# Performance work log

Hardware: AMD Instinct MI355X
Metric: run time of the kernel (lower is better)

The kernel has to match this reference:

```python
import jax, jax.numpy as jnp
import numpy as np

N = 50000
E = 800000
IN_C = 256
HID = 256
OUT_C = 128


def _glorot(key, fan_in, fan_out):
    lim = float(np.sqrt(6.0 / (fan_in + fan_out)))
    return jax.random.uniform(key, (fan_in, fan_out), jnp.float32, -lim, lim)


def setup_inputs() -> dict:
    key = jax.random.key(0)
    ks = jax.random.split(key, 10)
    x = jax.random.normal(ks[0], (N, IN_C), dtype=jnp.float32)
    edge_index = jax.random.randint(ks[1], (2, E), 0, N, dtype=jnp.int64)
    return {
        "x": x,
        "edge_index": edge_index,
        # layer 0 MLP: Linear(IN_C,HID)+ReLU+Linear(HID,HID)+ReLU
        "eps0": jnp.zeros((), jnp.float32),
        "W1_0": _glorot(ks[2], IN_C, HID),
        "b1_0": jnp.zeros((HID,), jnp.float32),
        "W2_0": _glorot(ks[3], HID, HID),
        "b2_0": jnp.zeros((HID,), jnp.float32),
        # layer 1 MLP: Linear(HID,HID)+ReLU+Linear(HID,OUT_C)
        "eps1": jnp.zeros((), jnp.float32),
        "W1_1": _glorot(ks[4], HID, HID),
        "b1_1": jnp.zeros((HID,), jnp.float32),
        "W2_1": _glorot(ks[5], HID, OUT_C),
        "b2_1": jnp.zeros((OUT_C,), jnp.float32),
    }


def _gin_layer(x, src, dst, eps, W1, b1, W2, b2, final_relu):
    # sum-aggregate messages x[src] into dst nodes
    agg = jax.ops.segment_sum(x[src], dst, num_segments=N)  # [N, d]
    h = (1.0 + eps) * x + agg
    h = jax.nn.relu(h @ W1 + b1)
    h = h @ W2 + b2
    return jax.nn.relu(h) if final_relu else h


def reference(x, edge_index, eps0, W1_0, b1_0, W2_0, b2_0, eps1, W1_1, b1_1, W2_1, b2_1):
    src, dst = edge_index[0], edge_index[1]
    h = _gin_layer(x, src, dst, eps0, W1_0, b1_0, W2_0, b2_0, final_relu=True)
    h = jax.nn.relu(h)  # model-level ReLU between layers
    h = _gin_layer(h, src, dst, eps1, W1_1, b1_1, W2_1, b2_1, final_relu=False)
    return jax.nn.log_softmax(h, axis=1)
```

## Files before the change

### kernel.cpp

```cpp
#include <hip/hip_runtime.h>

#define FDIM 256
#define OUTC 128
#define CAP  96
#define CURS 16
#define LDA 264
#define MROWS 64

typedef float floatx4 __attribute__((ext_vector_type(4)));
typedef __bf16 bf16x8 __attribute__((ext_vector_type(8)));

__device__ __forceinline__ unsigned short f2bf(float f) {
    union { float f; unsigned u; } v; v.f = f;
    unsigned r = v.u + 0x7FFF + ((v.u >> 16) & 1);
    return (unsigned short)(r >> 16);
}
__device__ __forceinline__ unsigned pack2(float a, float b) {
    return ((unsigned)f2bf(a)) | (((unsigned)f2bf(b)) << 16);
}
__device__ __forceinline__ unsigned q8b(float v, float rs) {
    int q = __float2int_rn(v * rs);
    q = (q < -127 ? -127 : (q > 127 ? 127 : q)) + 128;
    return (unsigned)q;
}
__device__ __forceinline__ float ub0(unsigned v) { float f; asm("v_cvt_f32_ubyte0 %0, %1" : "=v"(f) : "v"(v)); return f; }
__device__ __forceinline__ float ub1(unsigned v) { float f; asm("v_cvt_f32_ubyte1 %0, %1" : "=v"(f) : "v"(v)); return f; }
__device__ __forceinline__ float ub2(unsigned v) { float f; asm("v_cvt_f32_ubyte2 %0, %1" : "=v"(f) : "v"(v)); return f; }
__device__ __forceinline__ float ub3(unsigned v) { float f; asm("v_cvt_f32_ubyte3 %0, %1" : "=v"(f) : "v"(v)); return f; }

__device__ __forceinline__ void gl2lds16(const void* g, void* l) {
    __builtin_amdgcn_global_load_lds(
        (const __attribute__((address_space(1))) unsigned int*)g,
        (__attribute__((address_space(3))) unsigned int*)l, 16, 0, 0);
}

__global__ __launch_bounds__(256)
void prep_kernel(const int* __restrict__ src, const int* __restrict__ dst,
                 int* __restrict__ cursor, unsigned short* __restrict__ esrc2, int E,
                 const float* __restrict__ x, unsigned char* __restrict__ xq,
                 float* __restrict__ xs0, int total8,
                 const float* __restrict__ W1_0, const float* __restrict__ W2_0,
                 const float* __restrict__ W1_1, const float* __restrict__ W2_1,
                 unsigned short* __restrict__ w1f_0, unsigned short* __restrict__ w2f_0,
                 unsigned short* __restrict__ w1f_1, unsigned short* __restrict__ w2f_1) {
    int gid = blockIdx.x * 256 + threadIdx.x;
    if (gid < E) {
        int d = dst[gid];
        int pos = atomicAdd(&cursor[d * CURS], 1);
        if (pos < CAP) esrc2[d * CAP + pos] = (unsigned short)src[gid];
        return;
    }
    gid -= E;
    if (gid < total8) {
        const float4* p = (const float4*)(x + (size_t)gid * 8);
        float4 a = p[0], b = p[1];
        float m = fmaxf(fmaxf(fmaxf(fabsf(a.x), fabsf(a.y)), fmaxf(fabsf(a.z), fabsf(a.w))),
                        fmaxf(fmaxf(fabsf(b.x), fabsf(b.y)), fmaxf(fabsf(b.z), fabsf(b.w))));
        #pragma unroll
        for (int off = 1; off < 32; off <<= 1) m = fmaxf(m, __shfl_xor(m, off));
        float rs = (m > 0.f) ? 127.0f / m : 0.f;
        unsigned lo = q8b(a.x, rs) | (q8b(a.y, rs) << 8) |
                      (q8b(a.z, rs) << 16) | (q8b(a.w, rs) << 24);
        unsigned hi = q8b(b.x, rs) | (q8b(b.y, rs) << 8) |
                      (q8b(b.z, rs) << 16) | (q8b(b.w, rs) << 24);
        *(uint2*)(xq + (size_t)gid * 8) = make_uint2(lo, hi);
        if ((threadIdx.x & 31) == 0) xs0[gid >> 5] = m * (1.0f / 127.0f);
        return;
    }
    gid -= total8;
    const int S = FDIM * FDIM;
    const float* W; unsigned short* WF; int local, J, Ncols;
    if (gid < S)          { W = W1_0; WF = w1f_0; local = gid;         J = 4; Ncols = FDIM; }
    else if (gid < 2 * S) { W = W2_0; WF = w2f_0; local = gid - S;     J = 4; Ncols = FDIM; }
    else if (gid < 3 * S) { W = W1_1; WF = w1f_1; local = gid - 2 * S; J = 4; Ncols = FDIM; }
    else if (gid < 3 * S + FDIM * OUTC)
                          { W = W2_1; WF = w2f_1; local = gid - 3 * S; J = 2; Ncols = OUTC; }
    else return;
    int e    = local & 7;
    int lane = (local >> 3) & 63;
    int l15  = lane & 15;
    int quad = lane >> 4;
    int t  = local >> 9;
    int j  = t % J;  t /= J;
    int g  = t & 3;
    int kc = t >> 2;
    int n = g * (16 * J) + j * 16 + l15;
    int k = kc * 32 + quad * 8 + e;
    WF[local] = f2bf(W[(size_t)k * Ncols + n]);
}

__global__ __launch_bounds__(256)
void gather_q8_kernel(const unsigned char* __restrict__ q,
                      const float* __restrict__ qs,
                      const unsigned short* __restrict__ esrc2,
                      const int* __restrict__ cursor,
                      const float* __restrict__ epsp,
                      unsigned short* __restrict__ out, int N, float bias) {
    int node = __builtin_amdgcn_readfirstlane(
        (int)((blockIdx.x * blockDim.x + threadIdx.x) >> 6));
    int lane = threadIdx.x & 63;
    if (node >= N) return;
    int col = lane * 4;
    int beg = node * CAP;
    int cnt = cursor[node * CURS];
    if (cnt > CAP) cnt = CAP;

    float a4[4] = {0.f, 0.f, 0.f, 0.f};
    float scl_sum = 0.f;

    int e = 0;
    for (; e + 16 <= cnt; e += 16) {
        const uint4* ip = (const uint4*)(esrc2 + beg + e);
        uint4 i0 = ip[0], i1 = ip[1];
        unsigned iw[8] = {i0.x, i0.y, i0.z, i0.w, i1.x, i1.y, i1.z, i1.w};
        int s[16]; float sc[16];
        #pragma unroll
        for (int m = 0; m < 8; ++m) {
            s[2*m]   = __builtin_amdgcn_readfirstlane((int)(iw[m] & 0xffffu));
            s[2*m+1] = __builtin_amdgcn_readfirstlane((int)(iw[m] >> 16));
        }
        #pragma unroll
        for (int k = 0; k < 16; ++k) { sc[k] = qs[s[k]]; scl_sum += sc[k]; }
        unsigned v[16];
        #pragma unroll
        for (int k = 0; k < 16; ++k)
            v[k] = *(const unsigned*)(q + (size_t)s[k] * FDIM + col);
        #pragma unroll
        for (int k = 0; k < 16; ++k) {
            a4[0] = fmaf(sc[k], ub0(v[k]), a4[0]);
            a4[1] = fmaf(sc[k], ub1(v[k]), a4[1]);
            a4[2] = fmaf(sc[k], ub2(v[k]), a4[2]);
            a4[3] = fmaf(sc[k], ub3(v[k]), a4[3]);
        }
    }
    int rem = cnt - e;
    if (rem > 0) {
        const uint4* ip = (const uint4*)(esrc2 + beg + e);
        uint4 i0 = ip[0], i1 = ip[1];
        unsigned iw[8] = {i0.x, i0.y, i0.z, i0.w, i1.x, i1.y, i1.z, i1.w};
        int s[16]; float sc[16];
        #pragma unroll
        for (int m = 0; m < 8; ++m) {
            s[2*m]   = __builtin_amdgcn_readfirstlane((int)(iw[m] & 0xffffu));
            s[2*m+1] = __builtin_amdgcn_readfirstlane((int)(iw[m] >> 16));
        }
        #pragma unroll
        for (int k = 0; k < 16; ++k) if (k >= rem) s[k] = s[0];
        #pragma unroll
        for (int k = 0; k < 16; ++k) {
            sc[k] = (k < rem) ? qs[s[k]] : 0.f;
            scl_sum += sc[k];
        }
        unsigned v[16];
        #pragma unroll
        for (int k = 0; k < 16; ++k)
            v[k] = *(const unsigned*)(q + (size_t)s[k] * FDIM + col);
        #pragma unroll
        for (int k = 0; k < 16; ++k) {
            a4[0] = fmaf(sc[k], ub0(v[k]), a4[0]);
            a4[1] = fmaf(sc[k], ub1(v[k]), a4[1]);
            a4[2] = fmaf(sc[k], ub2(v[k]), a4[2]);
            a4[3] = fmaf(sc[k], ub3(v[k]), a4[3]);
        }
    }

    float ssc = qs[node] * (1.0f + *epsp);
    scl_sum += ssc;
    unsigned sv = *(const unsigned*)(q + (size_t)node * FDIM + col);
    a4[0] = fmaf(ssc, ub0(sv), a4[0]);
    a4[1] = fmaf(ssc, ub1(sv), a4[1]);
    a4[2] = fmaf(ssc, ub2(sv), a4[2]);
    a4[3] = fmaf(ssc, ub3(sv), a4[3]);

    float corr = bias * scl_sum;
    a4[0] -= corr; a4[1] -= corr; a4[2] -= corr; a4[3] -= corr;

    uint2 o;
    o.x = pack2(a4[0], a4[1]);
    o.y = pack2(a4[2], a4[3]);
    *(uint2*)(out + (size_t)node * FDIM + col) = o;
}

template<bool FINAL>
__global__ __launch_bounds__(256, 2)
void mlp_fused_kernel(const unsigned short* __restrict__ A,
                      const unsigned short* __restrict__ W1F,
                      const float* __restrict__ b1,
                      const unsigned short* __restrict__ W2F,
                      const float* __restrict__ b2,
                      void* __restrict__ Out,
                      float* __restrict__ xsp, int M) {
    __shared__ unsigned short As[MROWS * LDA];
    __shared__ unsigned short Bs[2][8192];
    __shared__ float sred[MROWS * 4 * 2];

    int tid  = threadIdx.x;
    int wave = tid >> 6;
    int lane = tid & 63;
    int l15  = lane & 15;
    int quad = lane >> 4;
    int row0 = blockIdx.x * MROWS;

    auto stageB = [&](const unsigned short* WF, int kcs, int buf, int sliceB) {
        const char* gs = (const char*)WF + (size_t)kcs * sliceB;
        char* ls = (char*)Bs[buf];
        int myg = wave * 1024 + lane * 16;
        int myl = wave * 1024;
        for (int r = 0; r < (sliceB >> 12); ++r)
            gl2lds16(gs + r * 4096 + myg, ls + r * 4096 + myl);
    };

    #pragma unroll
    for (int i = 0; i < 8; ++i) {
        int idx = i * 256 + tid;
        int r = idx >> 5;
        int c = (idx & 31) * 8;
        uint4 v = make_uint4(0u, 0u, 0u, 0u);
        int gr = row0 + r;
        if (gr < M) v = *(const uint4*)(A + (size_t)gr * FDIM + c);
        *(uint4*)(As + r * LDA + c) = v;
    }
    int cur = 0;
    stageB(W1F, 0, 0, 16384);
    asm volatile("s_waitcnt vmcnt(0)" ::: "memory");
    __syncthreads();

    floatx4 zero = {0.f, 0.f, 0.f, 0.f};

    {
        floatx4 acc[4][4];
        #pragma unroll
        for (int i = 0; i < 4; ++i)
            #pragma unroll
            for (int j = 0; j < 4; ++j) acc[i][j] = zero;

        for (int kc = 0; kc < 8; ++kc) {
            if (kc < 7) stageB(W1F, kc + 1, cur ^ 1, 16384);
            const unsigned short* Bc = Bs[cur] + wave * 2048;
            bf16x8 bf[4], af[4];
            #pragma unroll
            for (int j = 0; j < 4; ++j)
                bf[j] = *(const bf16x8*)(Bc + j * 512 + lane * 8);
            int k = kc * 32;
            #pragma unroll
            for (int i = 0; i < 4; ++i)
                af[i] = *(const bf16x8*)(As + (i * 16 + l15) * LDA + k + quad * 8);
            #pragma unroll
            for (int i = 0; i < 4; ++i)
                #pragma unroll
                for (int j = 0; j < 4; ++j)
                    acc[i][j] = __builtin_amdgcn_mfma_f32_16x16x32_bf16(
                        af[i], bf[j], acc[i][j], 0, 0, 0);
            asm volatile("s_waitcnt vmcnt(0)" ::: "memory");
            __syncthreads();
            cur ^= 1;
        }

        stageB(W2F, 0, cur, FINAL ? 8192 : 16384);

        #pragma unroll
        for (int j = 0; j < 4; ++j) {
            int col = wave * 64 + j * 16 + l15;
            float bv = b1[col];
            #pragma unroll
            for (int i = 0; i < 4; ++i) {
                #pragma unroll
                for (int r = 0; r < 4; ++r) {
                    float v = fmaxf(acc[i][j][r] + bv, 0.f);
                    As[(i * 16 + quad * 4 + r) * LDA + col] = f2bf(v);
                }
            }
        }
    }
    asm volatile("s_waitcnt vmcnt(0)" ::: "memory");
    __syncthreads();

    if (!FINAL) {
        floatx4 acc[4][4];
        #pragma unroll
        for (int i = 0; i < 4; ++i)
            #pragma unroll
            for (int j = 0; j < 4; ++j) acc[i][j] = zero;

        for (int kc = 0; kc < 8; ++kc) {
            if (kc < 7) stageB(W2F, kc + 1, cur ^ 1, 16384);
            const unsigned short* Bc = Bs[cur] + wave * 2048;
            bf16x8 bf[4], af[4];
            #pragma unroll
            for (int j = 0; j < 4; ++j)
                bf[j] = *(const bf16x8*)(Bc + j * 512 + lane * 8);
            int k = kc * 32;
            #pragma unroll
            for (int i = 0; i < 4; ++i)
                af[i] = *(const bf16x8*)(As + (i * 16 + l15) * LDA + k + quad * 8);
            #pragma unroll
            for (int i = 0; i < 4; ++i)
                #pragma unroll
                for (int j = 0; j < 4; ++j)
                    acc[i][j] = __builtin_amdgcn_mfma_f32_16x16x32_bf16(
                        af[i], bf[j], acc[i][j], 0, 0, 0);
            asm volatile("s_waitcnt vmcnt(0)" ::: "memory");
            __syncthreads();
            cur ^= 1;
        }

        #pragma unroll
        for (int j = 0; j < 4; ++j) {
            float bv = b2[wave * 64 + j * 16 + l15];
            #pragma unroll
            for (int i = 0; i < 4; ++i)
                #pragma unroll
                for (int r = 0; r < 4; ++r)
                    acc[i][j][r] = fmaxf(acc[i][j][r] + bv, 0.f);
        }
        #pragma unroll
        for (int i = 0; i < 4; ++i) {
            #pragma unroll
            for (int r = 0; r < 4; ++r) {
                float m = fmaxf(fmaxf(acc[i][0][r], acc[i][1][r]),
                                fmaxf(acc[i][2][r], acc[i][3][r]));
                #pragma unroll
                for (int off = 1; off < 16; off <<= 1) m = fmaxf(m, __shfl_xor(m, off));
                int row = i * 16 + quad * 4 + r;
                if (l15 == 0) sred[row * 4 + wave] = m;
            }
        }
        __syncthreads();

        unsigned char* Bq = (unsigned char*)As;
        #pragma unroll
        for (int i = 0; i < 4; ++i) {
            #pragma unroll
            for (int r = 0; r < 4; ++r) {
                int row = i * 16 + quad * 4 + r;
                float Mr = fmaxf(fmaxf(sred[row * 4 + 0], sred[row * 4 + 1]),
                                 fmaxf(sred[row * 4 + 2], sred[row * 4 + 3]));
                float rs = (Mr > 0.f) ? 255.0f / Mr : 0.f;
                if (wave == 0 && l15 == 0 && row0 + row < M)
                    xsp[row0 + row] = Mr * (1.0f / 255.0f);
                #pragma unroll
                for (int j = 0; j < 4; ++j) {
                    int col = wave * 64 + j * 16 + l15;
                    Bq[row * FDIM + col] =
                        (unsigned char)__float2int_rn(acc[i][j][r] * rs);
                }
            }
        }
        __syncthreads();

        unsigned char* Oq = (unsigned char*)Out;
        #pragma unroll
        for (int it = 0; it < 4; ++it) {
            int u4 = it * 256 + tid;
            int r = u4 >> 4;
            int gr = row0 + r;
            if (gr < M) {
                uint4 v = *(uint4*)(Bq + u4 * 16);
                *(uint4*)(Oq + (size_t)gr * FDIM + (u4 & 15) * 16) = v;
            }
        }
    } else {
        floatx4 acc[4][2];
        #pragma unroll
        for (int i = 0; i < 4; ++i)
            #pragma unroll
            for (int j = 0; j < 2; ++j) acc[i][j] = zero;

        for (int kc = 0; kc < 8; ++kc) {
            if (kc < 7) stageB(W2F, kc + 1, cur ^ 1, 8192);
            const unsigned short* Bc = Bs[cur] + wave * 1024;
            bf16x8 bf[2], af[4];
            #pragma unroll
            for (int j = 0; j < 2; ++j)
                bf[j] = *(const bf16x8*)(Bc + j * 512 + lane * 8);
            int k = kc * 32;
            #pragma unroll
            for (int i = 0; i < 4; ++i)
                af[i] = *(const bf16x8*)(As + (i * 16 + l15) * LDA + k + quad * 8);
            #pragma unroll
            for (int i = 0; i < 4; ++i)
                #pragma unroll
                for (int j = 0; j < 2; ++j)
                    acc[i][j] = __builtin_amdgcn_mfma_f32_16x16x32_bf16(
                        af[i], bf[j], acc[i][j], 0, 0, 0);
            asm volatile("s_waitcnt vmcnt(0)" ::: "memory");
            __syncthreads();
            cur ^= 1;
        }

        #pragma unroll
        for (int j = 0; j < 2; ++j) {
            float bv = b2[wave * 32 + j * 16 + l15];
            #pragma unroll
            for (int i = 0; i < 4; ++i)
                #pragma unroll
                for (int r = 0; r < 4; ++r) acc[i][j][r] += bv;
        }

        float* smax = sred;
        float* ssum = sred + MROWS * 4;

        #pragma unroll
        for (int i = 0; i < 4; ++i) {
            #pragma unroll
            for (int r = 0; r < 4; ++r) {
                float m = fmaxf(acc[i][0][r], acc[i][1][r]);
                #pragma unroll
                for (int off = 1; off < 16; off <<= 1) m = fmaxf(m, __shfl_xor(m, off));
                int row = i * 16 + quad * 4 + r;
                if (l15 == 0) smax[row * 4 + wave] = m;
            }
        }
        __syncthreads();

        float Mloc[4][4];
        #pragma unroll
        for (int i = 0; i < 4; ++i) {
            #pragma unroll
            for (int r = 0; r < 4; ++r) {
                int row = i * 16 + quad * 4 + r;
                float Mr = fmaxf(fmaxf(smax[row * 4 + 0], smax[row * 4 + 1]),
                                 fmaxf(smax[row * 4 + 2], smax[row * 4 + 3]));
                Mloc[i][r] = Mr;
                float s = __expf(acc[i][0][r] - Mr) + __expf(acc[i][1][r] - Mr);
                #pragma unroll
                for (int off = 1; off < 16; off <<= 1) s += __shfl_xor(s, off);
                if (l15 == 0) ssum[row * 4 + wave] = s;
            }
        }
        __syncthreads();

        float* O = (float*)Out;
        #pragma unroll
        for (int i = 0; i < 4; ++i) {
            #pragma unroll
            for (int r = 0; r < 4; ++r) {
                int row = i * 16 + quad * 4 + r;
                int grow = row0 + row;
                if (grow < M) {
                    float lse = Mloc[i][r] +
                        __logf(ssum[row * 4 + 0] + ssum[row * 4 + 1] +
                               ssum[row * 4 + 2] + ssum[row * 4 + 3]);
                    #pragma unroll
                    for (int j = 0; j < 2; ++j) {
                        int col = wave * 32 + j * 16 + l15;
                        O[(size_t)grow * OUTC + col] = acc[i][j][r] - lse;
                    }
                }
            }
        }
    }
}

extern "C" void kernel_launch(void* const* d_in, const int* in_sizes, int n_in,
                              void* d_out, int out_size, void* d_ws, size_t ws_size,
                              hipStream_t stream) {
    const float* x    = (const float*)d_in[0];
    const int*   ei   = (const int*)d_in[1];
    const float* eps0 = (const float*)d_in[2];
    const float* W1_0 = (const float*)d_in[3];
    const float* b1_0 = (const float*)d_in[4];
    const float* W2_0 = (const float*)d_in[5];
    const float* b2_0 = (const float*)d_in[6];
    const float* eps1 = (const float*)d_in[7];
    const float* W1_1 = (const float*)d_in[8];
    const float* b1_1 = (const float*)d_in[9];
    const float* W2_1 = (const float*)d_in[10];
    const float* b2_1 = (const float*)d_in[11];
    float* out = (float*)d_out;

    const int N = in_sizes[0] / FDIM;
    const int E = in_sizes[1] / 2;
    const int* src = ei;
    const int* dst = ei + E;

    size_t buf_elems = (size_t)N * FDIM;
    unsigned short* agg   = (unsigned short*)d_ws;
    float*          xs0   = (float*)(agg + buf_elems);
    float*          xs1   = xs0 + N;
    int*            cursor= (int*)(xs1 + N);
    unsigned short* esrc2 = (unsigned short*)(cursor + (size_t)N * CURS);
    unsigned short* w1f_0 = esrc2 + (size_t)N * CAP;
    unsigned short* w2f_0 = w1f_0 + FDIM * FDIM;
    unsigned short* w1f_1 = w2f_0 + FDIM * FDIM;
    unsigned short* w2f_1 = w1f_1 + FDIM * FDIM;
    unsigned char*  xq    = (unsigned char*)(w2f_1 + FDIM * OUTC);
    unsigned char*  h2q   = xq + buf_elems;

    int gather_blocks = (N + 3) / 4;
    int mlp_blocks = (N + MROWS - 1) / MROWS;
    int total8 = (int)(buf_elems / 8);
    int wtot = 3 * FDIM * FDIM + FDIM * OUTC;
    int prep_threads = E + total8 + wtot;

    hipMemsetAsync(cursor, 0, (size_t)N * CURS * sizeof(int), stream);
    prep_kernel<<<(prep_threads + 255) / 256, 256, 0, stream>>>(
        src, dst, cursor, esrc2, E, x, xq, xs0, total8,
        W1_0, W2_0, W1_1, W2_1, w1f_0, w2f_0, w1f_1, w2f_1);

    gather_q8_kernel<<<gather_blocks, 256, 0, stream>>>(
        xq, xs0, esrc2, cursor, eps0, agg, N, 128.0f);
    mlp_fused_kernel<false><<<mlp_blocks, 256, 0, stream>>>(
        agg, w1f_0, b1_0, w2f_0, b2_0, h2q, xs1, N);

    gather_q8_kernel<<<gather_blocks, 256, 0, stream>>>(
        h2q, xs1, esrc2, cursor, eps1, agg, N, 0.0f);
    mlp_fused_kernel<true><<<mlp_blocks, 256, 0, stream>>>(
        agg, w1f_1, b1_1, w2f_1, b2_1, out, nullptr, N);
}
```

Before: 292.9 us.

## Fuse neighbor gather into MLP kernel, aggregating directly into shared memory

The per-node quantized gather is merged into the fused MLP kernel. Each wave aggregates 16 nodes' neighbor rows straight into the LDS A-tile, so the bf16 agg buffer no longer makes a round trip through global memory, and two launches per layer become one. The cost is less parallelism in the gather phase: 782 blocks of 4 waves each loop serially over 16 nodes, where before there were 12500 blocks. Launch bounds also drop the min-2-blocks hint, and the gather latency now sits in front of the MFMA work in every block.

```diff
diff --git a/kernel.cpp b/kernel.cpp
--- a/kernel.cpp
+++ b/kernel.cpp
@@ -89,107 +89,19 @@
     WF[local] = f2bf(W[(size_t)k * Ncols + n]);
 }
 
+template<bool FINAL>
 __global__ __launch_bounds__(256)
-void gather_q8_kernel(const unsigned char* __restrict__ q,
+void gin_fused_kernel(const unsigned char* __restrict__ q,
                       const float* __restrict__ qs,
                       const unsigned short* __restrict__ esrc2,
                       const int* __restrict__ cursor,
                       const float* __restrict__ epsp,
-                      unsigned short* __restrict__ out, int N, float bias) {
-    int node = __builtin_amdgcn_readfirstlane(
-        (int)((blockIdx.x * blockDim.x + threadIdx.x) >> 6));
-    int lane = threadIdx.x & 63;
-    if (node >= N) return;
-    int col = lane * 4;
-    int beg = node * CAP;
-    int cnt = cursor[node * CURS];
-    if (cnt > CAP) cnt = CAP;
-
-    float a4[4] = {0.f, 0.f, 0.f, 0.f};
-    float scl_sum = 0.f;
-
-    int e = 0;
-    for (; e + 16 <= cnt; e += 16) {
-        const uint4* ip = (const uint4*)(esrc2 + beg + e);
-        uint4 i0 = ip[0], i1 = ip[1];
-        unsigned iw[8] = {i0.x, i0.y, i0.z, i0.w, i1.x, i1.y, i1.z, i1.w};
-        int s[16]; float sc[16];
-        #pragma unroll
-        for (int m = 0; m < 8; ++m) {
-            s[2*m]   = __builtin_amdgcn_readfirstlane((int)(iw[m] & 0xffffu));
-            s[2*m+1] = __builtin_amdgcn_readfirstlane((int)(iw[m] >> 16));
-        }
-        #pragma unroll
-        for (int k = 0; k < 16; ++k) { sc[k] = qs[s[k]]; scl_sum += sc[k]; }
-        unsigned v[16];
-        #pragma unroll
-        for (int k = 0; k < 16; ++k)
-            v[k] = *(const unsigned*)(q + (size_t)s[k] * FDIM + col);
-        #pragma unroll
-        for (int k = 0; k < 16; ++k) {
-            a4[0] = fmaf(sc[k], ub0(v[k]), a4[0]);
-            a4[1] = fmaf(sc[k], ub1(v[k]), a4[1]);
-            a4[2] = fmaf(sc[k], ub2(v[k]), a4[2]);
-            a4[3] = fmaf(sc[k], ub3(v[k]), a4[3]);
-        }
-    }
-    int rem = cnt - e;
-    if (rem > 0) {
-        const uint4* ip = (const uint4*)(esrc2 + beg + e);
-        uint4 i0 = ip[0], i1 = ip[1];
-        unsigned iw[8] = {i0.x, i0.y, i0.z, i0.w, i1.x, i1.y, i1.z, i1.w};
-        int s[16]; float sc[16];
-        #pragma unroll
-        for (int m = 0; m < 8; ++m) {
-            s[2*m]   = __builtin_amdgcn_readfirstlane((int)(iw[m] & 0xffffu));
-            s[2*m+1] = __builtin_amdgcn_readfirstlane((int)(iw[m] >> 16));
-        }
-        #pragma unroll
-        for (int k = 0; k < 16; ++k) if (k >= rem) s[k] = s[0];
-        #pragma unroll
-        for (int k = 0; k < 16; ++k) {
-            sc[k] = (k < rem) ? qs[s[k]] : 0.f;
-            scl_sum += sc[k];
-        }
-        unsigned v[16];
-        #pragma unroll
-        for (int k = 0; k < 16; ++k)
-            v[k] = *(const unsigned*)(q + (size_t)s[k] * FDIM + col);
-        #pragma unroll
-        for (int k = 0; k < 16; ++k) {
-            a4[0] = fmaf(sc[k], ub0(v[k]), a4[0]);
-            a4[1] = fmaf(sc[k], ub1(v[k]), a4[1]);
-            a4[2] = fmaf(sc[k], ub2(v[k]), a4[2]);
-            a4[3] = fmaf(sc[k], ub3(v[k]), a4[3]);
-        }
-    }
-
-    float ssc = qs[node] * (1.0f + *epsp);
-    scl_sum += ssc;
-    unsigned sv = *(const unsigned*)(q + (size_t)node * FDIM + col);
-    a4[0] = fmaf(ssc, ub0(sv), a4[0]);
-    a4[1] = fmaf(ssc, ub1(sv), a4[1]);
-    a4[2] = fmaf(ssc, ub2(sv), a4[2]);
-    a4[3] = fmaf(ssc, ub3(sv), a4[3]);
-
-    float corr = bias * scl_sum;
-    a4[0] -= corr; a4[1] -= corr; a4[2] -= corr; a4[3] -= corr;
-
-    uint2 o;
-    o.x = pack2(a4[0], a4[1]);
-    o.y = pack2(a4[2], a4[3]);
-    *(uint2*)(out + (size_t)node * FDIM + col) = o;
-}
-
-template<bool FINAL>
-__global__ __launch_bounds__(256, 2)
-void mlp_fused_kernel(const unsigned short* __restrict__ A,
                       const unsigned short* __restrict__ W1F,
                       const float* __restrict__ b1,
                       const unsigned short* __restrict__ W2F,
                       const float* __restrict__ b2,
                       void* __restrict__ Out,
-                      float* __restrict__ xsp, int M) {
+                      float* __restrict__ xsp, int N, float bias) {
     __shared__ unsigned short As[MROWS * LDA];
     __shared__ unsigned short Bs[2][8192];
     __shared__ float sred[MROWS * 4 * 2];
@@ -210,18 +122,94 @@
             gl2lds16(gs + r * 4096 + myg, ls + r * 4096 + myl);
     };
 
-    #pragma unroll
-    for (int i = 0; i < 8; ++i) {
-        int idx = i * 256 + tid;
-        int r = idx >> 5;
-        int c = (idx & 31) * 8;
-        uint4 v = make_uint4(0u, 0u, 0u, 0u);
-        int gr = row0 + r;
-        if (gr < M) v = *(const uint4*)(A + (size_t)gr * FDIM + c);
-        *(uint4*)(As + r * LDA + c) = v;
+    stageB(W1F, 0, 0, 16384);
+
+    float eps1p = 1.0f + *epsp;
+
+    int col = lane * 4;
+    for (int i = 0; i < 16; ++i) {
+        int lrow = wave * 16 + i;
+        int node = row0 + lrow;
+        float a4[4] = {0.f, 0.f, 0.f, 0.f};
+        if (node < N) {
+            int beg = node * CAP;
+            int cnt = cursor[node * CURS];
+            if (cnt > CAP) cnt = CAP;
+            float scl_sum = 0.f;
+
+            int e = 0;
+            for (; e + 16 <= cnt; e += 16) {
+                const uint4* ip = (const uint4*)(esrc2 + beg + e);
+                uint4 i0 = ip[0], i1 = ip[1];
+                unsigned iw[8] = {i0.x, i0.y, i0.z, i0.w, i1.x, i1.y, i1.z, i1.w};
+                int s[16]; float sc[16];
+                #pragma unroll
+                for (int m = 0; m < 8; ++m) {
+                    s[2*m]   = __builtin_amdgcn_readfirstlane((int)(iw[m] & 0xffffu));
+                    s[2*m+1] = __builtin_amdgcn_readfirstlane((int)(iw[m] >> 16));
+                }
+                #pragma unroll
+                for (int k = 0; k < 16; ++k) { sc[k] = qs[s[k]]; scl_sum += sc[k]; }
+                unsigned v[16];
+                #pragma unroll
+                for (int k = 0; k < 16; ++k)
+                    v[k] = *(const unsigned*)(q + (size_t)s[k] * FDIM + col);
+                #pragma unroll
+                for (int k = 0; k < 16; ++k) {
+                    a4[0] = fmaf(sc[k], ub0(v[k]), a4[0]);
+                    a4[1] = fmaf(sc[k], ub1(v[k]), a4[1]);
+                    a4[2] = fmaf(sc[k], ub2(v[k]), a4[2]);
+                    a4[3] = fmaf(sc[k], ub3(v[k]), a4[3]);
+                }
+            }
+            int rem = cnt - e;
+            if (rem > 0) {
+                const uint4* ip = (const uint4*)(esrc2 + beg + e);
+                uint4 i0 = ip[0], i1 = ip[1];
+                unsigned iw[8] = {i0.x, i0.y, i0.z, i0.w, i1.x, i1.y, i1.z, i1.w};
+                int s[16]; float sc[16];
+                #pragma unroll
+                for (int m = 0; m < 8; ++m) {
+                    s[2*m]   = __builtin_amdgcn_readfirstlane((int)(iw[m] & 0xffffu));
+                    s[2*m+1] = __builtin_amdgcn_readfirstlane((int)(iw[m] >> 16));
+                }
+                #pragma unroll
+                for (int k = 0; k < 16; ++k) if (k >= rem) s[k] = s[0];
+                #pragma unroll
+                for (int k = 0; k < 16; ++k) {
+                    sc[k] = (k < rem) ? qs[s[k]] : 0.f;
+                    scl_sum += sc[k];
+                }
+                unsigned v[16];
+                #pragma unroll
+                for (int k = 0; k < 16; ++k)
+                    v[k] = *(const unsigned*)(q + (size_t)s[k] * FDIM + col);
+                #pragma unroll
+                for (int k = 0; k < 16; ++k) {
+                    a4[0] = fmaf(sc[k], ub0(v[k]), a4[0]);
+                    a4[1] = fmaf(sc[k], ub1(v[k]), a4[1]);
+                    a4[2] = fmaf(sc[k], ub2(v[k]), a4[2]);
+                    a4[3] = fmaf(sc[k], ub3(v[k]), a4[3]);
+                }
+            }
+
+            float ssc = qs[node] * eps1p;
+            scl_sum += ssc;
+            unsigned sv = *(const unsigned*)(q + (size_t)node * FDIM + col);
+            a4[0] = fmaf(ssc, ub0(sv), a4[0]);
+            a4[1] = fmaf(ssc, ub1(sv), a4[1]);
+            a4[2] = fmaf(ssc, ub2(sv), a4[2]);
+            a4[3] = fmaf(ssc, ub3(sv), a4[3]);
+
+            float corr = bias * scl_sum;
+            a4[0] -= corr; a4[1] -= corr; a4[2] -= corr; a4[3] -= corr;
+        }
+        uint2 o;
+        o.x = pack2(a4[0], a4[1]);
+        o.y = pack2(a4[2], a4[3]);
+        *(uint2*)(As + lrow * LDA + col) = o;
     }
     int cur = 0;
-    stageB(W1F, 0, 0, 16384);
     asm volatile("s_waitcnt vmcnt(0)" ::: "memory");
     __syncthreads();
 
@@ -260,14 +248,14 @@
 
         #pragma unroll
         for (int j = 0; j < 4; ++j) {
-            int col = wave * 64 + j * 16 + l15;
-            float bv = b1[col];
+            int colw = wave * 64 + j * 16 + l15;
+            float bv = b1[colw];
             #pragma unroll
             for (int i = 0; i < 4; ++i) {
                 #pragma unroll
                 for (int r = 0; r < 4; ++r) {
                     float v = fmaxf(acc[i][j][r] + bv, 0.f);
-                    As[(i * 16 + quad * 4 + r) * LDA + col] = f2bf(v);
+                    As[(i * 16 + quad * 4 + r) * LDA + colw] = f2bf(v);
                 }
             }
         }
@@ -336,12 +324,12 @@
                 float Mr = fmaxf(fmaxf(sred[row * 4 + 0], sred[row * 4 + 1]),
                                  fmaxf(sred[row * 4 + 2], sred[row * 4 + 3]));
                 float rs = (Mr > 0.f) ? 255.0f / Mr : 0.f;
-                if (wave == 0 && l15 == 0 && row0 + row < M)
+                if (wave == 0 && l15 == 0 && row0 + row < N)
                     xsp[row0 + row] = Mr * (1.0f / 255.0f);
                 #pragma unroll
                 for (int j = 0; j < 4; ++j) {
-                    int col = wave * 64 + j * 16 + l15;
-                    Bq[row * FDIM + col] =
+                    int colw = wave * 64 + j * 16 + l15;
+                    Bq[row * FDIM + colw] =
                         (unsigned char)__float2int_rn(acc[i][j][r] * rs);
                 }
             }
@@ -354,7 +342,7 @@
             int u4 = it * 256 + tid;
             int r = u4 >> 4;
             int gr = row0 + r;
-            if (gr < M) {
+            if (gr < N) {
                 uint4 v = *(uint4*)(Bq + u4 * 16);
                 *(uint4*)(Oq + (size_t)gr * FDIM + (u4 & 15) * 16) = v;
             }
@@ -437,14 +425,14 @@
             for (int r = 0; r < 4; ++r) {
                 int row = i * 16 + quad * 4 + r;
                 int grow = row0 + row;
-                if (grow < M) {
+                if (grow < N) {
                     float lse = Mloc[i][r] +
                         __logf(ssum[row * 4 + 0] + ssum[row * 4 + 1] +
                                ssum[row * 4 + 2] + ssum[row * 4 + 3]);
                     #pragma unroll
                     for (int j = 0; j < 2; ++j) {
-                        int col = wave * 32 + j * 16 + l15;
-                        O[(size_t)grow * OUTC + col] = acc[i][j][r] - lse;
+                        int colw = wave * 32 + j * 16 + l15;
+                        O[(size_t)grow * OUTC + colw] = acc[i][j][r] - lse;
                     }
                 }
             }
@@ -475,8 +463,7 @@
     const int* dst = ei + E;
 
     size_t buf_elems = (size_t)N * FDIM;
-    unsigned short* agg   = (unsigned short*)d_ws;
-    float*          xs0   = (float*)(agg + buf_elems);
+    float*          xs0   = (float*)d_ws;
     float*          xs1   = xs0 + N;
     int*            cursor= (int*)(xs1 + N);
     unsigned short* esrc2 = (unsigned short*)(cursor + (size_t)N * CURS);
@@ -487,8 +474,7 @@
     unsigned char*  xq    = (unsigned char*)(w2f_1 + FDIM * OUTC);
     unsigned char*  h2q   = xq + buf_elems;
 
-    int gather_blocks = (N + 3) / 4;
-    int mlp_blocks = (N + MROWS - 1) / MROWS;
+    int fused_blocks = (N + MROWS - 1) / MROWS;
     int total8 = (int)(buf_elems / 8);
     int wtot = 3 * FDIM * FDIM + FDIM * OUTC;
     int prep_threads = E + total8 + wtot;
@@ -498,13 +484,9 @@
         src, dst, cursor, esrc2, E, x, xq, xs0, total8,
         W1_0, W2_0, W1_1, W2_1, w1f_0, w2f_0, w1f_1, w2f_1);
 
-    gather_q8_kernel<<<gather_blocks, 256, 0, stream>>>(
-        xq, xs0, esrc2, cursor, eps0, agg, N, 128.0f);
-    mlp_fused_kernel<false><<<mlp_blocks, 256, 0, stream>>>(
-        agg, w1f_0, b1_0, w2f_0, b2_0, h2q, xs1, N);
-
-    gather_q8_kernel<<<gather_blocks, 256, 0, stream>>>(
-        h2q, xs1, esrc2, cursor, eps1, agg, N, 0.0f);
-    mlp_fused_kernel<true><<<mlp_blocks, 256, 0, stream>>>(
-        agg, w1f_1, b1_1, w2f_1, b2_1, out, nullptr, N);
-}
+    gin_fused_kernel<false><<<fused_blocks, 256, 0, stream>>>(
+        xq, xs0, esrc2, cursor, eps0, w1f_0, b1_0, w2f_0, b2_0, h2q, xs1, N, 128.0f);
+
+    gin_fused_kernel<true><<<fused_blocks, 256, 0, stream>>>(
+        h2q, xs1, esrc2, cursor, eps1, w1f_1, b1_1, w2f_1, b2_1, out, nullptr, N, 0.0f);
+}
```

Result: slower. 376.4 us (+28.5%).
